# Optimization experiments

Hardware: AMD Instinct MI355X
Metric: run time of the kernel (lower is better)

Reference implementation:

```python
import jax, jax.numpy as jnp
import numpy as np

# Static config (matches init_kwargs)
B = 1; Z = 64; H = 64; W = 64; C = 96
NH = 3; WS = 4; SS = 2
N = WS ** 3                      # tokens per 3D window = 64
NW = (Z // WS) * (H // WS) * (W // WS)   # num windows = 4096
SCALE = (C // NH) ** -0.5
EPS = 1e-5


def _rel_pos_index():
    # same construction as WindowAttention3D.__init__ (torch.meshgrid default 'ij')
    coords = np.stack(np.meshgrid(np.arange(WS), np.arange(WS), np.arange(WS), indexing='ij'))
    cf = coords.reshape(3, -1)                       # (3, N)
    rc = (cf[:, :, None] - cf[:, None, :]).transpose(1, 2, 0)  # (N, N, 3)
    rc[:, :, 0] += WS - 1; rc[:, :, 1] += WS - 1; rc[:, :, 2] += WS - 1
    rc[:, :, 0] *= (2 * WS - 1) ** 2
    rc[:, :, 1] *= (2 * WS - 1)
    return rc.sum(-1)                                # (N, N) int


def _attn_mask():
    # shifted-window mask, as in SwinTransformerBlock3D.__init__
    img = np.zeros((Z, H, W), dtype=np.float32)
    sl = (slice(0, -WS), slice(-WS, -SS), slice(-SS, None))
    cnt = 0
    for z in sl:
        for h in sl:
            for w in sl:
                img[z, h, w] = cnt
                cnt += 1
    mw = img.reshape(Z // WS, WS, H // WS, WS, W // WS, WS)
    mw = mw.transpose(0, 2, 4, 1, 3, 5).reshape(-1, N)        # (nW, N)
    am = mw[:, None, :] - mw[:, :, None]                      # (nW, N, N)
    return np.where(am != 0, np.float32(-100.0), np.float32(0.0))


REL_IDX = jnp.asarray(_rel_pos_index())        # (N, N) int32, closed-over constant
ATTN_MASK = jnp.asarray(_attn_mask())          # (nW, N, N) float32


def _layernorm(x, g, b):
    m = x.mean(-1, keepdims=True)
    v = ((x - m) ** 2).mean(-1, keepdims=True)
    return (x - m) * jax.lax.rsqrt(v + EPS) * g + b


def _window_partition(x):
    # (B, Z, H, W, C) -> (B*nW, N, C)
    x = x.reshape(B, Z // WS, WS, H // WS, WS, W // WS, WS, C)
    return x.transpose(0, 1, 3, 5, 2, 4, 6, 7).reshape(-1, N, C)


def _window_reverse(wins):
    # (B*nW, N, C) -> (B, Z, H, W, C)
    x = wins.reshape(B, Z // WS, H // WS, W // WS, WS, WS, WS, C)
    return x.transpose(0, 1, 4, 2, 5, 3, 6, 7).reshape(B, Z, H, W, C)


def setup_inputs() -> dict:
    key = jax.random.key(0)
    ks = jax.random.split(key, 8)
    d = {
        'x': jax.random.normal(ks[0], (B, Z * H * W, C), jnp.float32),
        'norm1_w': jnp.ones((C,), jnp.float32),
        'norm1_b': jnp.zeros((C,), jnp.float32),
        'qkv_w': jax.random.normal(ks[1], (3 * C, C), jnp.float32) * 0.02,
        'qkv_b': jnp.zeros((3 * C,), jnp.float32),
        'rel_bias': jax.random.normal(ks[2], ((2 * WS - 1) ** 3, NH), jnp.float32) * 0.02,
        'proj_w': jax.random.normal(ks[3], (C, C), jnp.float32) * 0.02,
        'proj_b': jnp.zeros((C,), jnp.float32),
        'norm2_w': jnp.ones((C,), jnp.float32),
        'norm2_b': jnp.zeros((C,), jnp.float32),
        'fc1_w': jax.random.normal(ks[4], (4 * C, C), jnp.float32) * 0.02,
        'fc1_b': jnp.zeros((4 * C,), jnp.float32),
        'fc2_w': jax.random.normal(ks[5], (C, 4 * C), jnp.float32) * 0.02,
        'fc2_b': jnp.zeros((C,), jnp.float32),
    }
    return d


def reference(x, norm1_w, norm1_b, qkv_w, qkv_b, rel_bias, proj_w, proj_b,
              norm2_w, norm2_b, fc1_w, fc1_b, fc2_w, fc2_b):
    shortcut = x
    h = _layernorm(x, norm1_w, norm1_b).reshape(B, Z, H, W, C)
    # cyclic shift (SW-MSA)
    h = jnp.roll(h, (-SS, -SS, -SS), axis=(1, 2, 3))
    xw = _window_partition(h)                                  # (B*nW, N, C)
    qkv = (xw @ qkv_w.T + qkv_b).reshape(-1, N, 3, NH, C // NH)
    qkv = qkv.transpose(2, 0, 3, 1, 4)                         # (3, B_, NH, N, hd)
    q, k, v = qkv[0] * SCALE, qkv[1], qkv[2]
    attn = jnp.einsum('bhnd,bhmd->bhnm', q, k)                 # (B_, NH, N, N)
    bias = rel_bias[REL_IDX.reshape(-1)].reshape(N, N, NH).transpose(2, 0, 1)
    attn = attn + bias[None]
    attn = attn.reshape(B, NW, NH, N, N) + ATTN_MASK[None, :, None]
    attn = jax.nn.softmax(attn.reshape(-1, NH, N, N), axis=-1)
    out = jnp.einsum('bhnm,bhmd->bhnd', attn, v)
    out = out.transpose(0, 2, 1, 3).reshape(-1, N, C)
    out = out @ proj_w.T + proj_b
    h = _window_reverse(out)
    h = jnp.roll(h, (SS, SS, SS), axis=(1, 2, 3)).reshape(B, Z * H * W, C)
    x = shortcut + h                                            # residual (drop_path=0)
    y = _layernorm(x, norm2_w, norm2_b)
    y = jax.nn.gelu(y @ fc1_w.T + fc1_b, approximate=False)
    y = y @ fc2_w.T + fc2_b
    return x + y
```

## Files before the change

### kernel.cpp

```cpp
#include <hip/hip_runtime.h>

typedef __attribute__((ext_vector_type(8))) short short8;
typedef __attribute__((ext_vector_type(4))) float f32x4;

static __device__ __forceinline__ unsigned short f2bf(float f) {
  return (unsigned short)((__builtin_bit_cast(unsigned int, f) + 0x8000u) >> 16);
}
static __device__ __forceinline__ float bf2f(unsigned short u) {
  return __builtin_bit_cast(float, ((unsigned)u) << 16);
}
static __device__ __forceinline__ unsigned cvtpk(float a, float b) {
  unsigned r;
  asm("v_cvt_pk_bf16_f32 %0, %1, %2" : "=v"(r) : "v"(a), "v"(b));
  return r;
}

constexpr float LOG2E = 1.4426950408889634f;
constexpr float QSCL = 0.17677669529663687f * LOG2E;
constexpr int XP = 104;
constexpr int KP = 104;
constexpr int VTP = 72;

static __device__ __forceinline__ int frag_src(int o, int K) {
  const int j = o & 7;
  const int lane = (o >> 3) & 63;
  const int f = o >> 9;
  const int nks = K >> 5;
  const int ks = f % nks;
  const int t = f / nks;
  const int row = t * 16 + (lane & 15);
  const int k = ks * 32 + (lane >> 4) * 8 + j;
  return row * K + k;
}

__global__ void prep_kernel(const float* __restrict__ qkvw, const float* __restrict__ projw,
                            const float* __restrict__ fc1w, const float* __restrict__ fc2w,
                            const float* __restrict__ relbias,
                            unsigned short* __restrict__ ws, float* __restrict__ tab) {
  int i = blockIdx.x * 256 + threadIdx.x;
  if (i < 27648) ws[i] = f2bf(qkvw[frag_src(i, 96)]);
  if (i < 9216)  ws[27648 + i] = f2bf(projw[frag_src(i, 96)]);
  if (i < 36864) {
    ws[36864 + i] = f2bf(fc1w[frag_src(i, 96)]);
    ws[73728 + i] = f2bf(fc2w[frag_src(i, 384)]);
  }
  if (i < 98304) {
    const int r = i & 3, kgi = (i >> 2) & 3, q = (i >> 4) & 63, nt = (i >> 10) & 3;
    const int vh = i >> 12;
    const int h = vh % 3, v = vh / 3;
    const int key = nt * 16 + kgi * 4 + r;
    const bool bz = v & 4, bh = v & 2, bw = v & 1;
    const int iz = q >> 4, ih = (q >> 2) & 3, iw = q & 3;
    const int jz = key >> 4, jh = (key >> 2) & 3, jw = key & 3;
    const int idx = (iz - jz + 3) * 49 + (ih - jh + 3) * 7 + (iw - jw + 3);
    const int ci = (bz ? (iz < 2 ? 9 : 18) : 0) + (bh ? (ih < 2 ? 3 : 6) : 0) +
                   (bw ? (iw < 2 ? 1 : 2) : 0);
    const int cj = (bz ? (jz < 2 ? 9 : 18) : 0) + (bh ? (jh < 2 ? 3 : 6) : 0) +
                   (bw ? (jw < 2 ? 1 : 2) : 0);
    tab[i] = (relbias[idx * 3 + h] + (ci != cj ? -100.f : 0.f)) * LOG2E;
  }
}

__global__ __launch_bounds__(256, 3) void fused_kernel(
    const float* __restrict__ x,
    const float* __restrict__ n1w, const float* __restrict__ n1b,
    const float* __restrict__ qkvb, const float* __restrict__ tab,
    const float* __restrict__ projb,
    const float* __restrict__ n2w, const float* __restrict__ n2b,
    const float* __restrict__ b1, const float* __restrict__ b2,
    const unsigned short* __restrict__ wq, const unsigned short* __restrict__ wp,
    const unsigned short* __restrict__ w1, const unsigned short* __restrict__ w2,
    float* __restrict__ out) {
  __shared__ unsigned short Xo[64 * XP];
  __shared__ unsigned short Kb[64 * KP];
  __shared__ unsigned short Vt[96 * VTP];

  const int tid = threadIdx.x;
  const int bid = blockIdx.x;
  const int wz = bid >> 8, wh = (bid >> 4) & 15, ww = bid & 15;
  const int wave = tid >> 6, lane = tid & 63;
  const int ln = lane & 15, kg = lane >> 4;

  {
    const int n = tid >> 2, part = tid & 3;
    const int lz = n >> 4, lh = (n >> 2) & 3, lw = n & 3;
    const int sz = (wz * 4 + lz + 2) & 63;
    const int sh = (wh * 4 + lh + 2) & 63;
    const int sw = (ww * 4 + lw + 2) & 63;
    const float* px = x + (size_t)((sz * 64 + sh) * 64 + sw) * 96 + part * 24;
    float4 v[6];
#pragma unroll
    for (int j = 0; j < 6; ++j) v[j] = ((const float4*)px)[j];
    float s = 0.f, sq = 0.f;
#pragma unroll
    for (int j = 0; j < 6; ++j) {
      s += v[j].x + v[j].y + v[j].z + v[j].w;
      sq += v[j].x * v[j].x + v[j].y * v[j].y + v[j].z * v[j].z + v[j].w * v[j].w;
    }
    s += __shfl_xor(s, 1);  s += __shfl_xor(s, 2);
    sq += __shfl_xor(sq, 1); sq += __shfl_xor(sq, 2);
    const float mean = s * (1.f / 96.f);
    const float var = sq * (1.f / 96.f) - mean * mean;
    const float rs = rsqrtf(var + 1e-5f);
    const float4* g4 = (const float4*)(n1w + part * 24);
    const float4* b4 = (const float4*)(n1b + part * 24);
#pragma unroll
    for (int j = 0; j < 6; ++j) {
      float4 g = g4[j], b = b4[j];
      uint2 o;
      o.x = cvtpk((v[j].x - mean) * rs * g.x + b.x, (v[j].y - mean) * rs * g.y + b.y);
      o.y = cvtpk((v[j].z - mean) * rs * g.z + b.z, (v[j].w - mean) * rs * g.w + b.w);
      *(uint2*)&Xo[n * XP + part * 24 + j * 4] = o;
    }
  }

  short8 qa[3];
  {
    short8 a[3];
#pragma unroll
    for (int ks = 0; ks < 3; ++ks)
      a[ks] = *(const short8*)&Xo[(wave * 16 + ln) * XP + ks * 32 + kg * 8];
#pragma unroll
    for (int g = 0; g < 3; ++g) {
      short8 wf[6];
#pragma unroll
      for (int f = 0; f < 6; ++f)
        wf[f] = *(const short8*)&wq[(size_t)(g * 6 + f) * 512 + lane * 8];
#pragma unroll
      for (int t = 0; t < 2; ++t) {
        const int nt = g * 2 + t;
        const int oc = nt * 16 + ln;
        f32x4 acc = {0.f, 0.f, 0.f, 0.f};
#pragma unroll
        for (int ks = 0; ks < 3; ++ks)
          acc = __builtin_amdgcn_mfma_f32_16x16x32_bf16(a[ks], wf[t * 3 + ks], acc, 0, 0, 0);
        const float bias = qkvb[oc];
#pragma unroll
        for (int r = 0; r < 4; ++r)
          Kb[(wave * 16 + kg * 4 + r) * KP + oc] = f2bf((acc[r] + bias) * QSCL);
      }
    }
#pragma unroll
    for (int h = 0; h < 3; ++h)
      qa[h] = *(const short8*)&Kb[(wave * 16 + ln) * KP + h * 32 + kg * 8];
  }
  __syncthreads();

  {
    const int t0 = wave < 2 ? 6 + 2 * wave : 8 + wave;
    const int t1 = wave < 2 ? 7 + 2 * wave : 10 + 2 * wave;
    const int t2 = wave < 2 ? 12 + wave : 11 + 2 * wave;
#pragma unroll
    for (int i = 0; i < 3; ++i) {
      const int tile = i == 0 ? t0 : (i == 1 ? t1 : t2);
      const int oc = tile * 16 + ln;
      short8 wf[3];
#pragma unroll
      for (int ks = 0; ks < 3; ++ks)
        wf[ks] = *(const short8*)&wq[(size_t)(tile * 3 + ks) * 512 + lane * 8];
      const float bias = qkvb[oc];
#pragma unroll
      for (int rt = 0; rt < 4; ++rt) {
        f32x4 acc = {0.f, 0.f, 0.f, 0.f};
#pragma unroll
        for (int ks = 0; ks < 3; ++ks) {
          short8 a = *(const short8*)&Xo[(rt * 16 + ln) * XP + ks * 32 + kg * 8];
          acc = __builtin_amdgcn_mfma_f32_16x16x32_bf16(a, wf[ks], acc, 0, 0, 0);
        }
        if (tile < 12) {
#pragma unroll
          for (int r = 0; r < 4; ++r)
            Kb[(rt * 16 + kg * 4 + r) * KP + (tile - 12 + 6) * 16 + ln] = f2bf(acc[r] + bias);
        } else {
          uint2 u;
          u.x = cvtpk(acc[0] + bias, acc[1] + bias);
          u.y = cvtpk(acc[2] + bias, acc[3] + bias);
          *(uint2*)&Vt[((tile - 12) * 16 + ln) * VTP + rt * 16 + kg * 4] = u;
        }
      }
    }
  }
  __syncthreads();

  const int vv = ((wz == 15) ? 4 : 0) | ((wh == 15) ? 2 : 0) | ((ww == 15) ? 1 : 0);
  const float* tb0 = tab + (size_t)(vv * 3) * 4096;
  const int rowbase = wave * 16 + kg * 4;
  const int lA = ((kg & 1) << 5) + ln;
  const int lB = lA + 16;
#pragma unroll
  for (int h = 0; h < 3; ++h) {
    const float* tb = tb0 + h * 4096;
    f32x4 e[4];
#pragma unroll
    for (int nt = 0; nt < 4; ++nt) {
      short8 kf = *(const short8*)&Kb[(nt * 16 + ln) * KP + h * 32 + kg * 8];
      f32x4 trow = *(const f32x4*)(tb + nt * 1024 + (wave * 16 + ln) * 16 + kg * 4);
      f32x4 z = {0.f, 0.f, 0.f, 0.f};
      f32x4 st = __builtin_amdgcn_mfma_f32_16x16x32_bf16(kf, qa[h], z, 0, 0, 0);
#pragma unroll
      for (int r = 0; r < 4; ++r)
        e[nt][r] = __builtin_amdgcn_exp2f(st[r] + trow[r]);
    }
    float hs = 0.f;
#pragma unroll
    for (int nt = 0; nt < 4; ++nt)
#pragma unroll
      for (int r = 0; r < 4; ++r) hs += e[nt][r];
    hs += __shfl_xor(hs, 16);
    hs += __shfl_xor(hs, 32);
    const float inv = __builtin_amdgcn_rcpf(hs);
    unsigned pp[4][2];
#pragma unroll
    for (int nt = 0; nt < 4; ++nt) {
      pp[nt][0] = cvtpk(e[nt][0] * inv, e[nt][1] * inv);
      pp[nt][1] = cvtpk(e[nt][2] * inv, e[nt][3] * inv);
    }
    short8 paf[2];
#pragma unroll
    for (int ks = 0; ks < 2; ++ks) {
      const unsigned a0 = __shfl((int)pp[2 * ks][0], lA);
      const unsigned a1 = __shfl((int)pp[2 * ks][1], lA);
      const unsigned a2 = __shfl((int)pp[2 * ks][0], lB);
      const unsigned a3 = __shfl((int)pp[2 * ks][1], lB);
      const unsigned b0 = __shfl((int)pp[2 * ks + 1][0], lA);
      const unsigned b1 = __shfl((int)pp[2 * ks + 1][1], lA);
      const unsigned b2 = __shfl((int)pp[2 * ks + 1][0], lB);
      const unsigned b3 = __shfl((int)pp[2 * ks + 1][1], lB);
      const bool hi = (kg >> 1) != 0;
      uint4 wv;
      wv.x = hi ? b0 : a0;
      wv.y = hi ? b1 : a1;
      wv.z = hi ? b2 : a2;
      wv.w = hi ? b3 : a3;
      paf[ks] = __builtin_bit_cast(short8, wv);
    }
#pragma unroll
    for (int dt = 0; dt < 2; ++dt) {
      f32x4 oacc = {0.f, 0.f, 0.f, 0.f};
#pragma unroll
      for (int ks = 0; ks < 2; ++ks) {
        short8 vb = *(const short8*)&Vt[(h * 32 + dt * 16 + ln) * VTP + ks * 32 + kg * 8];
        oacc = __builtin_amdgcn_mfma_f32_16x16x32_bf16(paf[ks], vb, oacc, 0, 0, 0);
      }
#pragma unroll
      for (int r = 0; r < 4; ++r)
        Xo[(rowbase + r) * XP + h * 32 + dt * 16 + ln] = f2bf(oacc[r]);
    }
  }
  __syncthreads();

  unsigned short* X2b = Vt;

  {
    int gtok[4];
#pragma unroll
    for (int r = 0; r < 4; ++r) {
      const int n = rowbase + r;
      const int lz = n >> 4, lh = (n >> 2) & 3, lw = n & 3;
      const int oz = (wz * 4 + lz + 2) & 63;
      const int oh = (wh * 4 + lh + 2) & 63;
      const int ow = (ww * 4 + lw + 2) & 63;
      gtok[r] = (oz * 64 + oh) * 64 + ow;
    }
    short8 oa[3];
#pragma unroll
    for (int ks = 0; ks < 3; ++ks)
      oa[ks] = *(const short8*)&Xo[(wave * 16 + ln) * XP + ks * 32 + kg * 8];
    float s_[4] = {0.f, 0.f, 0.f, 0.f}, sq_[4] = {0.f, 0.f, 0.f, 0.f};
#pragma unroll
    for (int g = 0; g < 3; ++g) {
      short8 wf[6];
#pragma unroll
      for (int f = 0; f < 6; ++f)
        wf[f] = *(const short8*)&wp[(size_t)(g * 6 + f) * 512 + lane * 8];
#pragma unroll
      for (int t = 0; t < 2; ++t) {
        const int nt = g * 2 + t;
        const int col = nt * 16 + ln;
        f32x4 acc = {0.f, 0.f, 0.f, 0.f};
#pragma unroll
        for (int ks = 0; ks < 3; ++ks)
          acc = __builtin_amdgcn_mfma_f32_16x16x32_bf16(oa[ks], wf[t * 3 + ks], acc, 0, 0, 0);
        const float pbv = projb[col];
#pragma unroll
        for (int r = 0; r < 4; ++r) {
          const float v = x[(size_t)gtok[r] * 96 + col] + acc[r] + pbv;
          s_[r] += v;
          sq_[r] += v * v;
          X2b[(rowbase + r) * XP + col] = f2bf(v);
        }
      }
    }
#pragma unroll
    for (int r = 0; r < 4; ++r) {
      float s = s_[r], sq = sq_[r];
      s += __shfl_xor(s, 1);  s += __shfl_xor(s, 2);
      s += __shfl_xor(s, 4);  s += __shfl_xor(s, 8);
      sq += __shfl_xor(sq, 1); sq += __shfl_xor(sq, 2);
      sq += __shfl_xor(sq, 4); sq += __shfl_xor(sq, 8);
      const float mean = s * (1.f / 96.f);
      const float var = sq * (1.f / 96.f) - mean * mean;
      const float rs = rsqrtf(var + 1e-5f);
      s_[r] = mean;
      sq_[r] = rs;
    }
#pragma unroll
    for (int nt = 0; nt < 6; ++nt) {
      const int col = nt * 16 + ln;
      const float gw = n2w[col], gb = n2b[col];
#pragma unroll
      for (int r = 0; r < 4; ++r) {
        const float v = bf2f(X2b[(rowbase + r) * XP + col]);
        const float xl = (v - s_[r]) * sq_[r] * gw + gb;
        Xo[(rowbase + r) * XP + col] = f2bf(xl);
      }
    }
  }

  const int nf1 = (wave < 2) ? 1 : 2;
  const int f1base = (wave < 2) ? wave : 2 + 2 * (wave - 2);
  const int nf2 = (wave < 2) ? 2 : 1;
  const int f2base = (wave < 2) ? 2 * wave : 2 + wave;
  f32x4 acc2[2][4];
#pragma unroll
  for (int i = 0; i < 2; ++i)
#pragma unroll
    for (int rt = 0; rt < 4; ++rt) acc2[i][rt] = (f32x4){0.f, 0.f, 0.f, 0.f};

#pragma unroll 1
  for (int c = 0; c < 4; ++c) {
    __syncthreads();
#pragma unroll
    for (int i = 0; i < 2; ++i) {
      if (i < nf1) {
        const int tile = f1base + i;
        short8 wf1[3];
#pragma unroll
        for (int ks = 0; ks < 3; ++ks)
          wf1[ks] = *(const short8*)&w1[(size_t)(c * 18 + tile * 3 + ks) * 512 + lane * 8];
        const float bb = b1[c * 96 + tile * 16 + ln];
#pragma unroll
        for (int rt = 0; rt < 4; ++rt) {
          f32x4 acc = {0.f, 0.f, 0.f, 0.f};
#pragma unroll
          for (int ks = 0; ks < 3; ++ks) {
            short8 a = *(const short8*)&Xo[(rt * 16 + ln) * XP + ks * 32 + kg * 8];
            acc = __builtin_amdgcn_mfma_f32_16x16x32_bf16(a, wf1[ks], acc, 0, 0, 0);
          }
#pragma unroll
          for (int r = 0; r < 4; ++r) {
            const float v = acc[r] + bb;
            const float t2 = v * v;
            float p = fmaf(0.004287f, t2, -0.05694f);
            p = fmaf(p, t2, 0.3952f);
            float phi = fmaf(p, v, 0.5f);
            phi = fminf(fmaxf(phi, 0.f), 1.f);
            Kb[(rt * 16 + kg * 4 + r) * KP + tile * 16 + ln] = f2bf(v * phi);
          }
        }
      }
    }
    __syncthreads();
#pragma unroll
    for (int ks = 0; ks < 3; ++ks) {
      short8 wf2[2];
#pragma unroll
      for (int i = 0; i < 2; ++i)
        if (i < nf2)
          wf2[i] = *(const short8*)&w2[(size_t)((f2base + i) * 12 + c * 3 + ks) * 512 + lane * 8];
#pragma unroll
      for (int rt = 0; rt < 4; ++rt) {
        short8 pa = *(const short8*)&Kb[(rt * 16 + ln) * KP + ks * 32 + kg * 8];
#pragma unroll
        for (int i = 0; i < 2; ++i)
          if (i < nf2)
            acc2[i][rt] = __builtin_amdgcn_mfma_f32_16x16x32_bf16(pa, wf2[i], acc2[i][rt], 0, 0, 0);
      }
    }
  }

#pragma unroll
  for (int i = 0; i < 2; ++i) {
    if (i < nf2) {
      const int col = (f2base + i) * 16 + ln;
      const float bb = b2[col];
#pragma unroll
      for (int rt = 0; rt < 4; ++rt) {
#pragma unroll
        for (int r = 0; r < 4; ++r) {
          const int n = rt * 16 + kg * 4 + r;
          const int lz = n >> 4, lh = (n >> 2) & 3, lw = n & 3;
          const int oz = (wz * 4 + lz + 2) & 63;
          const int oh = (wh * 4 + lh + 2) & 63;
          const int ow = (ww * 4 + lw + 2) & 63;
          const size_t gt = (size_t)((oz * 64 + oh) * 64 + ow);
          const float v = bf2f(X2b[n * XP + col]);
          out[gt * 96 + col] = v + acc2[i][rt][r] + bb;
        }
      }
    }
  }
}

extern "C" void kernel_launch(void* const* d_in, const int* in_sizes, int n_in,
                              void* d_out, int out_size, void* d_ws, size_t ws_size,
                              hipStream_t stream) {
  const float* x    = (const float*)d_in[0];
  const float* n1w  = (const float*)d_in[1];
  const float* n1b  = (const float*)d_in[2];
  const float* qkvw = (const float*)d_in[3];
  const float* qkvb = (const float*)d_in[4];
  const float* relb = (const float*)d_in[5];
  const float* pw   = (const float*)d_in[6];
  const float* pb   = (const float*)d_in[7];
  const float* n2w  = (const float*)d_in[8];
  const float* n2b  = (const float*)d_in[9];
  const float* w1   = (const float*)d_in[10];
  const float* b1   = (const float*)d_in[11];
  const float* w2   = (const float*)d_in[12];
  const float* b2   = (const float*)d_in[13];
  float* out = (float*)d_out;

  unsigned short* wsq = (unsigned short*)d_ws;
  unsigned short* wsp = wsq + 27648;
  unsigned short* ws1 = wsp + 9216;
  unsigned short* ws2 = ws1 + 36864;
  float* tab = (float*)(wsq + 110592);

  hipLaunchKernelGGL(prep_kernel, dim3(384), dim3(256), 0, stream,
                     qkvw, pw, w1, w2, relb, wsq, tab);
  hipLaunchKernelGGL(fused_kernel, dim3(4096), dim3(256), 0, stream,
                     x, n1w, n1b, qkvb, tab, pb, n2w, n2b, b1, b2,
                     wsq, wsp, ws1, ws2, out);
}
```

Baseline: 139.0 us.

## Swap MFMA operands to produce transposed tiles for vectorized stores and loads

Swaps the A/B operands of several MFMA calls so each lane holds 4 consecutive output channels of one token rather than 4 tokens of one channel. This allows packed bf16 stores to LDS, float4 loads of residual and bias, and float4 global stores of the output. It also folds the Q scale into the prepacked weights and simplifies the LayerNorm reduction to two cross-lane shuffles per lane. The cost is different LDS bank access patterns and small bf16 rounding differences from pre-scaling Q weights.

```diff
diff --git a/kernel.cpp b/kernel.cpp
--- a/kernel.cpp
+++ b/kernel.cpp
@@ -6,8 +6,11 @@
 static __device__ __forceinline__ unsigned short f2bf(float f) {
   return (unsigned short)((__builtin_bit_cast(unsigned int, f) + 0x8000u) >> 16);
 }
-static __device__ __forceinline__ float bf2f(unsigned short u) {
-  return __builtin_bit_cast(float, ((unsigned)u) << 16);
+static __device__ __forceinline__ float bflo(unsigned u) {
+  return __builtin_bit_cast(float, u << 16);
+}
+static __device__ __forceinline__ float bfhi(unsigned u) {
+  return __builtin_bit_cast(float, u & 0xffff0000u);
 }
 static __device__ __forceinline__ unsigned cvtpk(float a, float b) {
   unsigned r;
@@ -38,7 +41,7 @@
                             const float* __restrict__ relbias,
                             unsigned short* __restrict__ ws, float* __restrict__ tab) {
   int i = blockIdx.x * 256 + threadIdx.x;
-  if (i < 27648) ws[i] = f2bf(qkvw[frag_src(i, 96)]);
+  if (i < 27648) ws[i] = f2bf(qkvw[frag_src(i, 96)] * (i < 9216 ? QSCL : 1.f));
   if (i < 9216)  ws[27648 + i] = f2bf(projw[frag_src(i, 96)]);
   if (i < 36864) {
     ws[36864 + i] = f2bf(fc1w[frag_src(i, 96)]);
@@ -80,6 +83,8 @@
   const int wz = bid >> 8, wh = (bid >> 4) & 15, ww = bid & 15;
   const int wave = tid >> 6, lane = tid & 63;
   const int ln = lane & 15, kg = lane >> 4;
+  const int oh_ = (wh * 4 + (ln >> 2) + 2) & 63;
+  const int ow_ = (ww * 4 + (ln & 3) + 2) & 63;
 
   {
     const int n = tid >> 2, part = tid & 3;
@@ -129,15 +134,15 @@
 #pragma unroll
       for (int t = 0; t < 2; ++t) {
         const int nt = g * 2 + t;
-        const int oc = nt * 16 + ln;
         f32x4 acc = {0.f, 0.f, 0.f, 0.f};
 #pragma unroll
         for (int ks = 0; ks < 3; ++ks)
-          acc = __builtin_amdgcn_mfma_f32_16x16x32_bf16(a[ks], wf[t * 3 + ks], acc, 0, 0, 0);
-        const float bias = qkvb[oc];
-#pragma unroll
-        for (int r = 0; r < 4; ++r)
-          Kb[(wave * 16 + kg * 4 + r) * KP + oc] = f2bf((acc[r] + bias) * QSCL);
+          acc = __builtin_amdgcn_mfma_f32_16x16x32_bf16(wf[t * 3 + ks], a[ks], acc, 0, 0, 0);
+        const float4 bq = *(const float4*)&qkvb[nt * 16 + kg * 4];
+        uint2 u;
+        u.x = cvtpk(fmaf(bq.x, QSCL, acc[0]), fmaf(bq.y, QSCL, acc[1]));
+        u.y = cvtpk(fmaf(bq.z, QSCL, acc[2]), fmaf(bq.w, QSCL, acc[3]));
+        *(uint2*)&Kb[(wave * 16 + ln) * KP + nt * 16 + kg * 4] = u;
       }
     }
 #pragma unroll
@@ -153,25 +158,35 @@
 #pragma unroll
     for (int i = 0; i < 3; ++i) {
       const int tile = i == 0 ? t0 : (i == 1 ? t1 : t2);
-      const int oc = tile * 16 + ln;
       short8 wf[3];
 #pragma unroll
       for (int ks = 0; ks < 3; ++ks)
         wf[ks] = *(const short8*)&wq[(size_t)(tile * 3 + ks) * 512 + lane * 8];
-      const float bias = qkvb[oc];
-#pragma unroll
-      for (int rt = 0; rt < 4; ++rt) {
-        f32x4 acc = {0.f, 0.f, 0.f, 0.f};
-#pragma unroll
-        for (int ks = 0; ks < 3; ++ks) {
-          short8 a = *(const short8*)&Xo[(rt * 16 + ln) * XP + ks * 32 + kg * 8];
-          acc = __builtin_amdgcn_mfma_f32_16x16x32_bf16(a, wf[ks], acc, 0, 0, 0);
+      if (tile < 12) {
+        const float4 bk = *(const float4*)&qkvb[tile * 16 + kg * 4];
+#pragma unroll
+        for (int rt = 0; rt < 4; ++rt) {
+          f32x4 acc = {0.f, 0.f, 0.f, 0.f};
+#pragma unroll
+          for (int ks = 0; ks < 3; ++ks) {
+            short8 a = *(const short8*)&Xo[(rt * 16 + ln) * XP + ks * 32 + kg * 8];
+            acc = __builtin_amdgcn_mfma_f32_16x16x32_bf16(wf[ks], a, acc, 0, 0, 0);
+          }
+          uint2 u;
+          u.x = cvtpk(acc[0] + bk.x, acc[1] + bk.y);
+          u.y = cvtpk(acc[2] + bk.z, acc[3] + bk.w);
+          *(uint2*)&Kb[(rt * 16 + ln) * KP + (tile - 6) * 16 + kg * 4] = u;
         }
-        if (tile < 12) {
-#pragma unroll
-          for (int r = 0; r < 4; ++r)
-            Kb[(rt * 16 + kg * 4 + r) * KP + (tile - 12 + 6) * 16 + ln] = f2bf(acc[r] + bias);
-        } else {
+      } else {
+        const float bias = qkvb[tile * 16 + ln];
+#pragma unroll
+        for (int rt = 0; rt < 4; ++rt) {
+          f32x4 acc = {0.f, 0.f, 0.f, 0.f};
+#pragma unroll
+          for (int ks = 0; ks < 3; ++ks) {
+            short8 a = *(const short8*)&Xo[(rt * 16 + ln) * XP + ks * 32 + kg * 8];
+            acc = __builtin_amdgcn_mfma_f32_16x16x32_bf16(a, wf[ks], acc, 0, 0, 0);
+          }
           uint2 u;
           u.x = cvtpk(acc[0] + bias, acc[1] + bias);
           u.y = cvtpk(acc[2] + bias, acc[3] + bias);
@@ -252,21 +267,13 @@
   unsigned short* X2b = Vt;
 
   {
-    int gtok[4];
-#pragma unroll
-    for (int r = 0; r < 4; ++r) {
-      const int n = rowbase + r;
-      const int lz = n >> 4, lh = (n >> 2) & 3, lw = n & 3;
-      const int oz = (wz * 4 + lz + 2) & 63;
-      const int oh = (wh * 4 + lh + 2) & 63;
-      const int ow = (ww * 4 + lw + 2) & 63;
-      gtok[r] = (oz * 64 + oh) * 64 + ow;
-    }
+    const int tok = wave * 16 + ln;
+    const int gt = ((wz * 4 + wave + 2) & 63) * 4096 + oh_ * 64 + ow_;
     short8 oa[3];
 #pragma unroll
     for (int ks = 0; ks < 3; ++ks)
-      oa[ks] = *(const short8*)&Xo[(wave * 16 + ln) * XP + ks * 32 + kg * 8];
-    float s_[4] = {0.f, 0.f, 0.f, 0.f}, sq_[4] = {0.f, 0.f, 0.f, 0.f};
+      oa[ks] = *(const short8*)&Xo[tok * XP + ks * 32 + kg * 8];
+    float s = 0.f, sq = 0.f;
 #pragma unroll
     for (int g = 0; g < 3; ++g) {
       short8 wf[6];
@@ -276,44 +283,40 @@
 #pragma unroll
       for (int t = 0; t < 2; ++t) {
         const int nt = g * 2 + t;
-        const int col = nt * 16 + ln;
         f32x4 acc = {0.f, 0.f, 0.f, 0.f};
 #pragma unroll
         for (int ks = 0; ks < 3; ++ks)
-          acc = __builtin_amdgcn_mfma_f32_16x16x32_bf16(oa[ks], wf[t * 3 + ks], acc, 0, 0, 0);
-        const float pbv = projb[col];
-#pragma unroll
-        for (int r = 0; r < 4; ++r) {
-          const float v = x[(size_t)gtok[r] * 96 + col] + acc[r] + pbv;
-          s_[r] += v;
-          sq_[r] += v * v;
-          X2b[(rowbase + r) * XP + col] = f2bf(v);
-        }
-      }
-    }
-#pragma unroll
-    for (int r = 0; r < 4; ++r) {
-      float s = s_[r], sq = sq_[r];
-      s += __shfl_xor(s, 1);  s += __shfl_xor(s, 2);
-      s += __shfl_xor(s, 4);  s += __shfl_xor(s, 8);
-      sq += __shfl_xor(sq, 1); sq += __shfl_xor(sq, 2);
-      sq += __shfl_xor(sq, 4); sq += __shfl_xor(sq, 8);
-      const float mean = s * (1.f / 96.f);
-      const float var = sq * (1.f / 96.f) - mean * mean;
-      const float rs = rsqrtf(var + 1e-5f);
-      s_[r] = mean;
-      sq_[r] = rs;
-    }
+          acc = __builtin_amdgcn_mfma_f32_16x16x32_bf16(wf[t * 3 + ks], oa[ks], acc, 0, 0, 0);
+        const float4 xr4 = *(const float4*)&x[(size_t)gt * 96 + nt * 16 + kg * 4];
+        const float4 pb4 = *(const float4*)&projb[nt * 16 + kg * 4];
+        const float v0 = xr4.x + acc[0] + pb4.x;
+        const float v1 = xr4.y + acc[1] + pb4.y;
+        const float v2 = xr4.z + acc[2] + pb4.z;
+        const float v3 = xr4.w + acc[3] + pb4.w;
+        s += v0 + v1 + v2 + v3;
+        sq += v0 * v0 + v1 * v1 + v2 * v2 + v3 * v3;
+        uint2 u;
+        u.x = cvtpk(v0, v1);
+        u.y = cvtpk(v2, v3);
+        *(uint2*)&X2b[tok * XP + nt * 16 + kg * 4] = u;
+      }
+    }
+    s += __shfl_xor(s, 16);  s += __shfl_xor(s, 32);
+    sq += __shfl_xor(sq, 16); sq += __shfl_xor(sq, 32);
+    const float mean = s * (1.f / 96.f);
+    const float var = sq * (1.f / 96.f) - mean * mean;
+    const float rs = rsqrtf(var + 1e-5f);
 #pragma unroll
     for (int nt = 0; nt < 6; ++nt) {
-      const int col = nt * 16 + ln;
-      const float gw = n2w[col], gb = n2b[col];
-#pragma unroll
-      for (int r = 0; r < 4; ++r) {
-        const float v = bf2f(X2b[(rowbase + r) * XP + col]);
-        const float xl = (v - s_[r]) * sq_[r] * gw + gb;
-        Xo[(rowbase + r) * XP + col] = f2bf(xl);
-      }
+      const uint2 u = *(const uint2*)&X2b[tok * XP + nt * 16 + kg * 4];
+      const float4 gw = *(const float4*)&n2w[nt * 16 + kg * 4];
+      const float4 gb = *(const float4*)&n2b[nt * 16 + kg * 4];
+      uint2 o;
+      o.x = cvtpk((bflo(u.x) - mean) * rs * gw.x + gb.x,
+                  (bfhi(u.x) - mean) * rs * gw.y + gb.y);
+      o.y = cvtpk((bflo(u.y) - mean) * rs * gw.z + gb.z,
+                  (bfhi(u.y) - mean) * rs * gw.w + gb.w);
+      *(uint2*)&Xo[tok * XP + nt * 16 + kg * 4] = o;
     }
   }
 
@@ -338,25 +341,31 @@
 #pragma unroll
         for (int ks = 0; ks < 3; ++ks)
           wf1[ks] = *(const short8*)&w1[(size_t)(c * 18 + tile * 3 + ks) * 512 + lane * 8];
-        const float bb = b1[c * 96 + tile * 16 + ln];
+        const float4 b14 = *(const float4*)&b1[c * 96 + tile * 16 + kg * 4];
 #pragma unroll
         for (int rt = 0; rt < 4; ++rt) {
           f32x4 acc = {0.f, 0.f, 0.f, 0.f};
 #pragma unroll
           for (int ks = 0; ks < 3; ++ks) {
             short8 a = *(const short8*)&Xo[(rt * 16 + ln) * XP + ks * 32 + kg * 8];
-            acc = __builtin_amdgcn_mfma_f32_16x16x32_bf16(a, wf1[ks], acc, 0, 0, 0);
+            acc = __builtin_amdgcn_mfma_f32_16x16x32_bf16(wf1[ks], a, acc, 0, 0, 0);
           }
+          float gl[4];
 #pragma unroll
           for (int r = 0; r < 4; ++r) {
-            const float v = acc[r] + bb;
+            const float bv = r == 0 ? b14.x : (r == 1 ? b14.y : (r == 2 ? b14.z : b14.w));
+            const float v = acc[r] + bv;
             const float t2 = v * v;
             float p = fmaf(0.004287f, t2, -0.05694f);
             p = fmaf(p, t2, 0.3952f);
             float phi = fmaf(p, v, 0.5f);
             phi = fminf(fmaxf(phi, 0.f), 1.f);
-            Kb[(rt * 16 + kg * 4 + r) * KP + tile * 16 + ln] = f2bf(v * phi);
+            gl[r] = v * phi;
           }
+          uint2 u;
+          u.x = cvtpk(gl[0], gl[1]);
+          u.y = cvtpk(gl[2], gl[3]);
+          *(uint2*)&Kb[(rt * 16 + ln) * KP + tile * 16 + kg * 4] = u;
         }
       }
     }
@@ -374,7 +383,7 @@
 #pragma unroll
         for (int i = 0; i < 2; ++i)
           if (i < nf2)
-            acc2[i][rt] = __builtin_amdgcn_mfma_f32_16x16x32_bf16(pa, wf2[i], acc2[i][rt], 0, 0, 0);
+            acc2[i][rt] = __builtin_amdgcn_mfma_f32_16x16x32_bf16(wf2[i], pa, acc2[i][rt], 0, 0, 0);
       }
     }
   }
@@ -382,21 +391,19 @@
 #pragma unroll
   for (int i = 0; i < 2; ++i) {
     if (i < nf2) {
-      const int col = (f2base + i) * 16 + ln;
-      const float bb = b2[col];
+      const int colb = (f2base + i) * 16 + kg * 4;
+      const float4 b24 = *(const float4*)&b2[colb];
 #pragma unroll
       for (int rt = 0; rt < 4; ++rt) {
-#pragma unroll
-        for (int r = 0; r < 4; ++r) {
-          const int n = rt * 16 + kg * 4 + r;
-          const int lz = n >> 4, lh = (n >> 2) & 3, lw = n & 3;
-          const int oz = (wz * 4 + lz + 2) & 63;
-          const int oh = (wh * 4 + lh + 2) & 63;
-          const int ow = (ww * 4 + lw + 2) & 63;
-          const size_t gt = (size_t)((oz * 64 + oh) * 64 + ow);
-          const float v = bf2f(X2b[n * XP + col]);
-          out[gt * 96 + col] = v + acc2[i][rt][r] + bb;
-        }
+        const int tok = rt * 16 + ln;
+        const size_t gt = (size_t)(((wz * 4 + rt + 2) & 63) * 4096 + oh_ * 64 + ow_);
+        const uint2 u = *(const uint2*)&X2b[tok * XP + colb];
+        float4 o;
+        o.x = bflo(u.x) + acc2[i][rt][0] + b24.x;
+        o.y = bfhi(u.x) + acc2[i][rt][1] + b24.y;
+        o.z = bflo(u.y) + acc2[i][rt][2] + b24.z;
+        o.w = bfhi(u.y) + acc2[i][rt][3] + b24.w;
+        *(float4*)&out[gt * 96 + colb] = o;
       }
     }
   }
```

Result: slower. 156.8 us (+12.8%).
